# Kernel tuning notes

Hardware: AMD Instinct MI355X
Metric: run time of the kernel (lower is better)

Reference implementation:

```python
import jax, jax.numpy as jnp
import numpy as np

N_NODES = 100000
N_EDGES = 1600000
IN_F = 256
OUT_F = 64
ALPHA = 0.2  # LeakyReLU negative slope


def setup_inputs() -> dict:
    key = jax.random.key(0)
    k1, k2, k3, k4 = jax.random.split(key, 4)
    x = jax.random.normal(k1, (N_NODES, IN_F), dtype=jnp.float32)
    indices = jax.random.randint(k2, (2, N_EDGES), 0, N_NODES, dtype=jnp.int64)
    # xavier_uniform with gain=1.414 ~ U(-b, b), b = gain*sqrt(6/(fan_in+fan_out))
    bW = 1.414 * np.sqrt(6.0 / (IN_F + OUT_F))
    W = jax.random.uniform(k3, (IN_F, OUT_F), dtype=jnp.float32, minval=-bW, maxval=bW)
    ba = 1.414 * np.sqrt(6.0 / (2 * OUT_F + 1))
    a = jax.random.uniform(k4, (2 * OUT_F, 1), dtype=jnp.float32, minval=-ba, maxval=ba)
    return {"x": x, "indices": indices, "W": W, "a": a}


def reference(x, indices, W, a):
    # h = X @ W  -> [N, F_out]
    h = x @ W
    N = h.shape[0]
    src = indices[0]  # segment ids (softmax rows / aggregation targets)
    dst = indices[1]  # gathered neighbor features

    # e_ij = leakyrelu([h_i || h_j] @ a) = leakyrelu(h_i@a1 + h_j@a2)
    # (identical math to concatenation, avoids materializing [E, 2F])
    a1 = a[:OUT_F, 0]
    a2 = a[OUT_F:, 0]
    s1 = h @ a1  # [N]
    s2 = h @ a2  # [N]
    logits = s1[src] + s2[dst]  # [E]
    e = jnp.where(logits > 0, logits, ALPHA * logits)

    # segment softmax over edges grouped by src (sp_softmax)
    m = jax.ops.segment_max(e, src, num_segments=N)
    ex = jnp.exp(e - m[src])
    denom = jax.ops.segment_sum(ex, src, num_segments=N)
    att = ex / denom[src]  # [E]

    # h_prime[i] = sum_j att_ij * h_j  (sp_matmul: weighted scatter-aggregate)
    h_prime = jax.ops.segment_sum(att[:, None] * h[dst], src, num_segments=N)

    # concat=True -> ELU
    return jax.nn.elu(h_prime)
```

## Files before the change

### kernel.cpp

```cpp
#include <hip/hip_runtime.h>
#include <hip/hip_bf16.h>
#include <math.h>

#define NN 100000
#define NE 1600000
#define INF_ 256
#define OF 64

#define NPB 128
#define NB  782
#define CAPB 2560
#define ED (CAPB + 128)
#define GEMMB 782
#define P1B 512
#define CH1 ((NE + P1B - 1) / P1B)
#define OVCAP 8192

constexpr float LRELU_ALPHA = 0.2f;

typedef __attribute__((ext_vector_type(8))) short short8;
typedef __attribute__((ext_vector_type(4))) float f32x4;

static __device__ __forceinline__ unsigned short f2bf(float f) {
    union { float f; unsigned int u; } v; v.f = f;
    unsigned int r = v.u + 0x7fff + ((v.u >> 16) & 1);
    return (unsigned short)(r >> 16);
}
static __device__ __forceinline__ float bf2f(unsigned short b) {
    union { unsigned int u; float f; } v; v.u = ((unsigned int)b) << 16;
    return v.f;
}
static __device__ __forceinline__ unsigned int pkbf(float a, float b) {
    union { __hip_bfloat162 h; unsigned int u; } c;
    c.h = __float22bfloat162_rn(make_float2(a, b));
    return c.u;
}

union S8 { short8 s; unsigned int u[4]; };

__global__ __launch_bounds__(256) void k_fused1(const float* __restrict__ x,
                                                const float* __restrict__ W,
                                                const float* __restrict__ a,
                                                const int* __restrict__ idx,
                                                int* __restrict__ cur_b,
                                                int* __restrict__ pairs,
                                                int2* __restrict__ ov_list,
                                                unsigned short* __restrict__ h,
                                                float* __restrict__ s1,
                                                float* __restrict__ s2) {
    __shared__ __align__(16) char smem[43008];
    int tid = threadIdx.x;

    if (blockIdx.x < GEMMB) {
        short* Wf  = (short*)smem;
        float* wal = (float*)(smem + 40960);

        {
            float t1 = 0.f, t2 = 0.f;
            const float* wr = W + tid * OF;
#pragma unroll 8
            for (int c = 0; c < OF; ++c) {
                float w = wr[c];
                t1 += w * a[c];
                t2 += w * a[OF + c];
            }
            wal[tid] = t1;
            wal[256 + tid] = t2;
        }
        __syncthreads();

        for (int i = tid; i < 2560; i += 256) {
            int ks = i / 320;
            int rem = i - ks * 320;
            int ct = rem >> 6;
            int l  = rem & 63;
            int kb = ks * 32 + ((l >> 4) << 3);
            int c  = l & 15;
            S8 v;
            if (ct < 4) {
                int col = ct * 16 + c;
#pragma unroll
                for (int j = 0; j < 4; ++j)
                    v.u[j] = pkbf(W[(size_t)(kb + 2 * j) * OF + col],
                                  W[(size_t)(kb + 2 * j + 1) * OF + col]);
            } else if (c < 2) {
                const float* src = wal + c * 256;
#pragma unroll
                for (int j = 0; j < 4; ++j)
                    v.u[j] = pkbf(src[kb + 2 * j], src[kb + 2 * j + 1]);
            } else {
#pragma unroll
                for (int j = 0; j < 4; ++j) v.u[j] = 0u;
            }
            ((short8*)Wf)[i] = v.s;
        }
        __syncthreads();

        int wid = tid >> 6, lane = tid & 63;
        int rowbase = blockIdx.x * 128 + wid * 32;
        int r0 = rowbase + (lane & 15);
        int koff = (lane >> 4) << 3;

        f32x4 acc[2][5];
#pragma unroll
        for (int rt = 0; rt < 2; ++rt)
#pragma unroll
            for (int ct = 0; ct < 5; ++ct) acc[rt][ct] = (f32x4){0.f, 0.f, 0.f, 0.f};

#pragma unroll 1
        for (int ks = 0; ks < 8; ++ks) {
            S8 af[2];
#pragma unroll
            for (int rt = 0; rt < 2; ++rt) {
                int r = r0 + rt * 16;
                if (r < NN) {
                    const float* p = x + (size_t)r * INF_ + ks * 32 + koff;
                    float4 xa = *(const float4*)p;
                    float4 xb = *(const float4*)(p + 4);
                    af[rt].u[0] = pkbf(xa.x, xa.y);
                    af[rt].u[1] = pkbf(xa.z, xa.w);
                    af[rt].u[2] = pkbf(xb.x, xb.y);
                    af[rt].u[3] = pkbf(xb.z, xb.w);
                } else {
#pragma unroll
                    for (int j = 0; j < 4; ++j) af[rt].u[j] = 0u;
                }
            }
#pragma unroll
            for (int rt = 0; rt < 2; ++rt)
#pragma unroll
                for (int ct = 0; ct < 5; ++ct)
                    acc[rt][ct] = __builtin_amdgcn_mfma_f32_16x16x32_bf16(
                        af[rt].s, ((short8*)Wf)[(ks * 5 + ct) * 64 + lane], acc[rt][ct], 0, 0, 0);
        }

        int c = lane & 15, rowq = lane >> 4;
#pragma unroll
        for (int rt = 0; rt < 2; ++rt) {
#pragma unroll
            for (int reg = 0; reg < 4; ++reg) {
                int r = rowbase + rt * 16 + rowq * 4 + reg;
                if (r < NN) {
#pragma unroll
                    for (int ct = 0; ct < 4; ++ct)
                        h[(size_t)r * OF + ct * 16 + c] = f2bf(acc[rt][ct][reg]);
                    float sv = acc[rt][4][reg];
                    if (c == 0)      s1[r] = sv;
                    else if (c == 1) s2[r] = sv;
                }
            }
        }
    } else {
        int blk = blockIdx.x - GEMMB;
        int* hist  = (int*)smem;
        int* gbase = (int*)smem + NB;
        for (int i = tid; i < NB; i += 256) hist[i] = 0;
        __syncthreads();
        int e0 = blk * CH1, e1 = min(e0 + CH1, NE);
        for (int e = e0 + tid; e < e1; e += 256)
            atomicAdd(&hist[idx[e] >> 7], 1);
        __syncthreads();
        for (int i = tid; i < NB; i += 256) {
            int c = hist[i];
            gbase[i] = c ? atomicAdd(&cur_b[i], c) : 0;
            hist[i] = 0;
        }
        __syncthreads();
        for (int e = e0 + tid; e < e1; e += 256) {
            int s = idx[e], d = idx[NE + e];
            int b = s >> 7;
            int p = gbase[b] + atomicAdd(&hist[b], 1);
            if (p < CAPB) pairs[b * CAPB + p] = ((s & 127) << 17) | d;
            else {
                int j = atomicAdd(&cur_b[NB], 1);
                if (j < OVCAP) ov_list[j] = make_int2(s, d);
            }
        }
    }
}

__global__ __launch_bounds__(256) void k_fused2(const int* __restrict__ pairs,
                                                const int* __restrict__ cur_b,
                                                const int2* __restrict__ ov_list,
                                                const float* __restrict__ s1,
                                                const float* __restrict__ s2,
                                                const unsigned short* __restrict__ h,
                                                float* __restrict__ out) {
    __shared__ int  stage[ED];
    __shared__ int2 el[ED];
    __shared__ int cnt[NPB], pfx[NPB], cur[NPB];
    __shared__ float s1l[NPB];
    __shared__ int extra;
    int tid = threadIdx.x, b = blockIdx.x;
    int node0 = b * NPB;

    if (tid < NPB) {
        cnt[tid] = 0;
        int g = node0 + tid;
        s1l[tid] = (g < NN) ? s1[g] : 0.f;
    }
    if (tid == 0) extra = 0;
    __syncthreads();

    int t_b = cur_b[b];
    int nin = min(t_b, CAPB);
    for (int i = tid; i < nin; i += 256) {
        int v = pairs[b * CAPB + i];
        stage[i] = v;
        atomicAdd(&cnt[v >> 17], 1);
    }
    if (t_b > CAPB) {
        int ovn = min(cur_b[NB], OVCAP);
        for (int i = tid; i < ovn; i += 256) {
            int2 e = ov_list[i];
            if ((e.x >> 7) == b) {
                int k = atomicAdd(&extra, 1);
                if (k < 128) {
                    stage[CAPB + k] = ((e.x & 127) << 17) | e.y;
                    atomicAdd(&cnt[e.x & 127], 1);
                }
            }
        }
    }
    __syncthreads();
    int ntot = nin + min(extra, 128);

    if (tid < NPB) pfx[tid] = cnt[tid];
    __syncthreads();
    for (int off = 1; off < NPB; off <<= 1) {
        int xv = (tid >= off && tid < NPB) ? pfx[tid - off] : 0;
        __syncthreads();
        if (tid < NPB) pfx[tid] += xv;
        __syncthreads();
    }
    if (tid < NPB) cur[tid] = pfx[tid] - cnt[tid];
    __syncthreads();

    for (int i = tid; i < ntot; i += 256) {
        int v = stage[i];
        int ls = v >> 17;
        int p = atomicAdd(&cur[ls], 1);
        el[p] = make_int2(v & 0x1FFFF, ls);
    }
    __syncthreads();

    for (int i = tid; i < ntot; i += 256) {
        int2 e = el[i];
        float lg = s1l[e.y] + s2[e.x];
        float elr = lg > 0.f ? lg : LRELU_ALPHA * lg;
        el[i].y = __float_as_int(expf(elr));
    }
    __syncthreads();

    int wid = tid >> 6, lane = tid & 63;
    int half = lane >> 5, f2 = lane & 31;
    for (int ln = wid * 32; ln < wid * 32 + 32; ++ln) {
        int node = node0 + ln;
        if (node >= NN) break;
        int dg = cnt[ln];
        int st = pfx[ln] - dg;
        float den = 0.f, ax = 0.f, ay = 0.f;
        for (int j = half; j < dg; j += 2) {
            int2 e = el[st + j];
            float ex = __int_as_float(e.y);
            den += ex;
            unsigned int hv = *(const unsigned int*)(h + (size_t)e.x * OF + f2 * 2);
            ax += ex * bf2f((unsigned short)(hv & 0xFFFFu));
            ay += ex * bf2f((unsigned short)(hv >> 16));
        }
        den += __shfl_xor(den, 32, 64);
        ax  += __shfl_xor(ax, 32, 64);
        ay  += __shfl_xor(ay, 32, 64);
        float inv = den > 0.f ? 1.f / den : 0.f;
        float vx = ax * inv, vy = ay * inv;
        vx = vx > 0.f ? vx : expf(vx) - 1.f;
        vy = vy > 0.f ? vy : expf(vy) - 1.f;
        if (half == 0)
            *(float2*)(out + (size_t)node * OF + f2 * 2) = make_float2(vx, vy);
    }
}

extern "C" void kernel_launch(void* const* d_in, const int* in_sizes, int n_in,
                              void* d_out, int out_size, void* d_ws, size_t ws_size,
                              hipStream_t stream) {
    const float* x   = (const float*)d_in[0];
    const int*   idx = (const int*)d_in[1];
    const float* W   = (const float*)d_in[2];
    const float* a   = (const float*)d_in[3];
    float* out = (float*)d_out;

    char* ws = (char*)d_ws;
    unsigned short* h = (unsigned short*)ws;  ws += sizeof(unsigned short) * (size_t)NN * OF;
    int*  pairs       = (int*)ws;             ws += sizeof(int) * (size_t)NB * CAPB;
    float* s1         = (float*)ws;           ws += sizeof(float) * NN;
    float* s2         = (float*)ws;           ws += sizeof(float) * NN;
    int*   cur_b      = (int*)ws;             ws += sizeof(int) * (NB + 16);
    int2*  ov_list    = (int2*)ws;            ws += sizeof(int2) * OVCAP;

    hipMemsetAsync(cur_b, 0, sizeof(int) * (NB + 16), stream);
    k_fused1<<<GEMMB + P1B, 256, 0, stream>>>(x, W, a, idx, cur_b, pairs, ov_list, h, s1, s2);
    k_fused2<<<NB, 256, 0, stream>>>(pairs, cur_b, ov_list, s1, s2, h, out);
}
```

Measured before the change: 343.4 us.

## Split edge partition and aggregation into separate kernels with per-node waves

The fused kernel that sorted edges and then aggregated 128 nodes per block is split in two. The first kernel sorts edges and writes sorted (dst, exp-logit) pairs plus per-node start and degree to global memory. The second kernel gives each wave one node across many small blocks, staging edges through shared memory. The intent is better load balance and occupancy during the gather-heavy aggregation, since the old kernel ran only 782 blocks with large shared memory. The cost is an extra launch and a global round trip for the sorted edge list, about 12.8 MB written and read back.

```diff
diff --git a/kernel.cpp b/kernel.cpp
--- a/kernel.cpp
+++ b/kernel.cpp
@@ -179,15 +179,15 @@
     }
 }
 
-__global__ __launch_bounds__(256) void k_fused2(const int* __restrict__ pairs,
-                                                const int* __restrict__ cur_b,
-                                                const int2* __restrict__ ov_list,
-                                                const float* __restrict__ s1,
-                                                const float* __restrict__ s2,
-                                                const unsigned short* __restrict__ h,
-                                                float* __restrict__ out) {
-    __shared__ int  stage[ED];
-    __shared__ int2 el[ED];
+__global__ __launch_bounds__(256) void k_part2(const int* __restrict__ pairs,
+                                               const int* __restrict__ cur_b,
+                                               const int2* __restrict__ ov_list,
+                                               const float* __restrict__ s1,
+                                               const float* __restrict__ s2,
+                                               int* __restrict__ start,
+                                               int* __restrict__ deg,
+                                               int2* __restrict__ el_g) {
+    __shared__ int stage[ED];
     __shared__ int cnt[NPB], pfx[NPB], cur[NPB];
     __shared__ float s1l[NPB];
     __shared__ int extra;
@@ -233,51 +233,69 @@
         if (tid < NPB) pfx[tid] += xv;
         __syncthreads();
     }
-    if (tid < NPB) cur[tid] = pfx[tid] - cnt[tid];
+    if (tid < NPB) {
+        int ex = pfx[tid] - cnt[tid];
+        int g = node0 + tid;
+        if (g < NN) { start[g] = b * CAPB + ex; deg[g] = cnt[tid]; }
+        cur[tid] = ex;
+    }
     __syncthreads();
-
     for (int i = tid; i < ntot; i += 256) {
         int v = stage[i];
-        int ls = v >> 17;
+        int ls = v >> 17, dst = v & 0x1FFFF;
         int p = atomicAdd(&cur[ls], 1);
-        el[p] = make_int2(v & 0x1FFFF, ls);
-    }
-    __syncthreads();
-
-    for (int i = tid; i < ntot; i += 256) {
-        int2 e = el[i];
-        float lg = s1l[e.y] + s2[e.x];
+        float lg = s1l[ls] + s2[dst];
         float elr = lg > 0.f ? lg : LRELU_ALPHA * lg;
-        el[i].y = __float_as_int(expf(elr));
-    }
-    __syncthreads();
-
+        el_g[b * CAPB + p] = make_int2(dst, __float_as_int(expf(elr)));
+    }
+}
+
+__global__ __launch_bounds__(256) void k_agg(const int2* __restrict__ el_g,
+                                             const int* __restrict__ start,
+                                             const int* __restrict__ deg,
+                                             const unsigned short* __restrict__ h,
+                                             float* __restrict__ out) {
+    __shared__ int2 tile[4][64];
+    int tid = threadIdx.x;
     int wid = tid >> 6, lane = tid & 63;
+    int node = blockIdx.x * 4 + wid;
+    if (node >= NN) return;
+
+    int st = start[node];
+    int dg = deg[node];
     int half = lane >> 5, f2 = lane & 31;
-    for (int ln = wid * 32; ln < wid * 32 + 32; ++ln) {
-        int node = node0 + ln;
-        if (node >= NN) break;
-        int dg = cnt[ln];
-        int st = pfx[ln] - dg;
-        float den = 0.f, ax = 0.f, ay = 0.f;
-        for (int j = half; j < dg; j += 2) {
-            int2 e = el[st + j];
+    float den = 0.f, ax = 0.f, ay = 0.f;
+
+    for (int base = 0; base < dg; base += 64) {
+        int cnt = min(64, dg - base);
+        if (lane < cnt) {
+            int2 pr = el_g[st + base + lane];
+            den += __int_as_float(pr.y);
+            tile[wid][lane] = pr;
+        }
+        asm volatile("s_waitcnt lgkmcnt(0)" ::: "memory");
+#pragma unroll 4
+        for (int j = half; j < cnt; j += 2) {
+            int2 e = tile[wid][j];
             float ex = __int_as_float(e.y);
-            den += ex;
             unsigned int hv = *(const unsigned int*)(h + (size_t)e.x * OF + f2 * 2);
             ax += ex * bf2f((unsigned short)(hv & 0xFFFFu));
             ay += ex * bf2f((unsigned short)(hv >> 16));
         }
-        den += __shfl_xor(den, 32, 64);
-        ax  += __shfl_xor(ax, 32, 64);
-        ay  += __shfl_xor(ay, 32, 64);
-        float inv = den > 0.f ? 1.f / den : 0.f;
-        float vx = ax * inv, vy = ay * inv;
-        vx = vx > 0.f ? vx : expf(vx) - 1.f;
-        vy = vy > 0.f ? vy : expf(vy) - 1.f;
-        if (half == 0)
-            *(float2*)(out + (size_t)node * OF + f2 * 2) = make_float2(vx, vy);
-    }
+        asm volatile("" ::: "memory");
+    }
+
+#pragma unroll
+    for (int off = 1; off < 64; off <<= 1) den += __shfl_xor(den, off, 64);
+    ax += __shfl_xor(ax, 32, 64);
+    ay += __shfl_xor(ay, 32, 64);
+
+    float inv = den > 0.f ? 1.f / den : 0.f;
+    float vx = ax * inv, vy = ay * inv;
+    vx = vx > 0.f ? vx : expf(vx) - 1.f;
+    vy = vy > 0.f ? vy : expf(vy) - 1.f;
+    if (half == 0)
+        *(float2*)(out + (size_t)node * OF + f2 * 2) = make_float2(vx, vy);
 }
 
 extern "C" void kernel_launch(void* const* d_in, const int* in_sizes, int n_in,
@@ -292,12 +310,16 @@
     char* ws = (char*)d_ws;
     unsigned short* h = (unsigned short*)ws;  ws += sizeof(unsigned short) * (size_t)NN * OF;
     int*  pairs       = (int*)ws;             ws += sizeof(int) * (size_t)NB * CAPB;
+    int2* el_g        = (int2*)ws;            ws += sizeof(int2) * (size_t)NB * CAPB;
     float* s1         = (float*)ws;           ws += sizeof(float) * NN;
     float* s2         = (float*)ws;           ws += sizeof(float) * NN;
+    int*   start      = (int*)ws;             ws += sizeof(int) * NN;
+    int*   deg        = (int*)ws;             ws += sizeof(int) * NN;
     int*   cur_b      = (int*)ws;             ws += sizeof(int) * (NB + 16);
     int2*  ov_list    = (int2*)ws;            ws += sizeof(int2) * OVCAP;
 
     hipMemsetAsync(cur_b, 0, sizeof(int) * (NB + 16), stream);
     k_fused1<<<GEMMB + P1B, 256, 0, stream>>>(x, W, a, idx, cur_b, pairs, ov_list, h, s1, s2);
-    k_fused2<<<NB, 256, 0, stream>>>(pairs, cur_b, ov_list, s1, s2, h, out);
-}
+    k_part2<<<NB, 256, 0, stream>>>(pairs, cur_b, ov_list, s1, s2, start, deg, el_g);
+    k_agg<<<(NN + 3) / 4, 256, 0, stream>>>(el_g, start, deg, h, out);
+}
```

After: 289.0 us. -15.8%, faster.
